# Kernel optimization log

Hardware: AMD Instinct MI355X
Metric: run time of the kernel (lower is better)

## Reference

```python
import jax, jax.numpy as jnp
import numpy as np

N, D, K = 10000, 784, 16          # nodes, input feat dim, num_neighbors
E = N * (K - 1)                   # edges
H = 128                           # hidden width in all MLPs
SIZES = [784, 128, 2]             # node_sizes


def setup_inputs() -> dict:
    key = jax.random.key(0)
    ks = jax.random.split(key, 24)
    w = lambda k, shape: jax.random.normal(k, shape, jnp.float32) * 0.02
    inp = {
        "x": jax.random.normal(ks[0], (N, D), jnp.float32),
        "edge_attr": jax.random.uniform(ks[1], (E, 1), jnp.float32),
        "idxs": jax.random.randint(ks[2], (N, K - 1), 0, N, dtype=jnp.int32),
    }
    # Layer 1: in=784, msg_size=784, out=128
    inp["l1_msg_w1"] = w(ks[3], (D + 1, H));      inp["l1_msg_b1"] = jnp.zeros((H,), jnp.float32)
    inp["l1_msg_w2"] = w(ks[4], (H, D));          inp["l1_msg_b2"] = jnp.zeros((D,), jnp.float32)
    inp["l1_node_w1"] = w(ks[5], (D + D, H));     inp["l1_node_b1"] = jnp.zeros((H,), jnp.float32)
    inp["l1_node_w2"] = w(ks[6], (H, 128));       inp["l1_node_b2"] = jnp.zeros((128,), jnp.float32)
    # Layer 2: in=128, msg_size=128, out=2
    inp["l2_msg_w1"] = w(ks[7], (128 + 1, H));    inp["l2_msg_b1"] = jnp.zeros((H,), jnp.float32)
    inp["l2_msg_w2"] = w(ks[8], (H, 128));        inp["l2_msg_b2"] = jnp.zeros((128,), jnp.float32)
    inp["l2_node_w1"] = w(ks[9], (128 + 128, H)); inp["l2_node_b1"] = jnp.zeros((H,), jnp.float32)
    inp["l2_node_w2"] = w(ks[10], (H, 2));        inp["l2_node_b2"] = jnp.zeros((2,), jnp.float32)
    return inp


def _mlp(x, w1, b1, w2, b2):
    return jax.nn.relu(x @ w1 + b1) @ w2 + b2


def _node_layer(x, src, edge_attr,
                mw1, mb1, mw2, mb2, nw1, nb1, nw2, nb2):
    # message over edges: cat(x[src], edge_attr) -> MLP   [E, msg_size]
    msg = _mlp(jnp.concatenate([x[src], edge_attr], axis=1), mw1, mb1, mw2, mb2)
    # scatter_mean by src index (faithful to the original, which uses index=src)
    sums = jax.ops.segment_sum(msg, src, num_segments=N)
    cnt = jax.ops.segment_sum(jnp.ones((src.shape[0], 1), msg.dtype), src, num_segments=N)
    agg = jnp.where(cnt > 0, sums / jnp.maximum(cnt, 1.0), 0.0)
    # node update: cat(x, agg_msg) -> MLP
    return _mlp(jnp.concatenate([x, agg], axis=1), nw1, nb1, nw2, nb2)


def reference(x, edge_attr, idxs,
              l1_msg_w1, l1_msg_b1, l1_msg_w2, l1_msg_b2,
              l1_node_w1, l1_node_b1, l1_node_w2, l1_node_b2,
              l2_msg_w1, l2_msg_b1, l2_msg_w2, l2_msg_b2,
              l2_node_w1, l2_node_b1, l2_node_w2, l2_node_b2):
    src = idxs.reshape(-1)  # [E]; dst is unused by the original message computation
    h = _node_layer(x, src, edge_attr,
                    l1_msg_w1, l1_msg_b1, l1_msg_w2, l1_msg_b2,
                    l1_node_w1, l1_node_b1, l1_node_w2, l1_node_b2)
    proj = _node_layer(h, src, edge_attr,
                       l2_msg_w1, l2_msg_b1, l2_msg_w2, l2_msg_b2,
                       l2_node_w1, l2_node_b1, l2_node_w2, l2_node_b2)  # [N, 2]
    # vectorized per-neighbor squared distances (replaces the nested python loop)
    neigh = proj[idxs]                                   # [N, K-1, 2]
    d = jnp.sum((proj[:, None, :] - neigh) ** 2, axis=-1)  # [N, K-1]
    return d.reshape(-1, 1)                              # [N*(K-1), 1]
```

## Files before the change

kernel.cpp:

```cpp
#include <hip/hip_runtime.h>

#define N_NODES 10000
#define E_EDGES 150000
#define KNB     15
#define EBLOCKS 587
#define GEMMB   1252
#define KPAD    800
#define PLSTR   204800

typedef unsigned short u16;
typedef __bf16 bf16x8 __attribute__((ext_vector_type(8)));
typedef float  f32x4  __attribute__((ext_vector_type(4)));

__device__ __forceinline__ void split3(float a, u16& h, u16& m, u16& l) {
    unsigned u = __float_as_uint(a);
    unsigned t = u + 0x7FFFu + ((u >> 16) & 1u);
    h = (u16)(t >> 16);
    float r1 = a - __uint_as_float(t & 0xFFFF0000u);
    unsigned u1 = __float_as_uint(r1);
    m = (u16)(u1 >> 16);
    float r2 = r1 - __uint_as_float(u1 & 0xFFFF0000u);
    l = (u16)(__float_as_uint(r2) >> 16);
}

__device__ __forceinline__ void gl_lds16(const u16* g, u16* l) {
    __builtin_amdgcn_global_load_lds(
        (const __attribute__((address_space(1))) unsigned int*)(g),
        (__attribute__((address_space(3))) unsigned int*)(l),
        16, 0, 0);
}

__global__ void count_kernel(const int* __restrict__ idxs, int* __restrict__ cnt, int e) {
    int i = blockIdx.x * blockDim.x + threadIdx.x;
    if (i < e) atomicAdd(&cnt[idxs[i]], 1);
}

__device__ __forceinline__
void gemm_tile2(const float* __restrict__ A, int K,
                const float* __restrict__ Blo, const float* __restrict__ Bhi, int ldB,
                float* __restrict__ C, int ldC, int M,
                int rowBlk, int colBlk) {
    __shared__ float As2[16][34];
    __shared__ float Bs2[16][64];
    int tid = threadIdx.x;
    int tn  = tid & 15, tm = tid >> 4;
    int arow = tid >> 3, acB = (tid & 7) << 1;
    int brow = tid >> 4, bcol = (tid & 15) << 2;
    int rowBase = rowBlk * 32, colBase = colBlk * 64;

    bool half = (Bhi != nullptr) && (colBase >= 128);
    const float* B = half ? Bhi : Blo;
    int bj = colBase - (half ? 128 : 0) + bcol;

    float2 av; float4 bv;
    auto loadA = [&](int k0, float2& dst) {
        int gr = rowBase + arow;
        if (gr < M) dst = *(const float2*)(A + (size_t)gr * K + k0 + acB);
        else { dst.x = dst.y = 0.f; }
    };
    auto loadB = [&](int k0, float4& dst) {
        dst = *(const float4*)(B + (size_t)(k0 + brow) * ldB + bj);
    };
    loadA(0, av); loadB(0, bv);

    float acc[2][4] = {};
    for (int k0 = 0; k0 < K; k0 += 16) {
        __syncthreads();
        As2[acB + 0][arow] = av.x; As2[acB + 1][arow] = av.y;
        *(float4*)&Bs2[brow][bcol] = bv;
        __syncthreads();
        if (k0 + 16 < K) { loadA(k0 + 16, av); loadB(k0 + 16, bv); }
#pragma unroll
        for (int k = 0; k < 16; ++k) {
            float4 b = *(const float4*)&Bs2[k][tn << 2];
            float2 a = *(const float2*)&As2[k][tm << 1];
            acc[0][0] = fmaf(a.x, b.x, acc[0][0]); acc[0][1] = fmaf(a.x, b.y, acc[0][1]);
            acc[0][2] = fmaf(a.x, b.z, acc[0][2]); acc[0][3] = fmaf(a.x, b.w, acc[0][3]);
            acc[1][0] = fmaf(a.y, b.x, acc[1][0]); acc[1][1] = fmaf(a.y, b.y, acc[1][1]);
            acc[1][2] = fmaf(a.y, b.z, acc[1][2]); acc[1][3] = fmaf(a.y, b.w, acc[1][3]);
        }
    }
#pragma unroll
    for (int i = 0; i < 2; ++i) {
        int row = rowBase + tm * 2 + i;
        if (row >= M) continue;
#pragma unroll
        for (int j = 0; j < 4; ++j)
            C[(size_t)row * ldC + colBase + (tn << 2) + j] = acc[i][j];
    }
}

__global__ __launch_bounds__(256)
void scanfold_kernel(const float* __restrict__ mw2, const float* __restrict__ mb2,
                     const float* __restrict__ nw1, const float* __restrict__ nb2,
                     const float* __restrict__ nw2,
                     const float* __restrict__ m2w1, const float* __restrict__ m2b1,
                     const float* __restrict__ m2w2, const float* __restrict__ m2b2,
                     const float* __restrict__ n2w1, const float* __restrict__ n2b1,
                     float* __restrict__ M1, float* __restrict__ M2,
                     float* __restrict__ WH,
                     float* __restrict__ v1, float* __restrict__ v2,
                     float* __restrict__ bu2, float* __restrict__ bx2,
                     const int* __restrict__ cnt, int* __restrict__ eoff,
                     float* __restrict__ maskv, int* __restrict__ fillc,
                     const float* __restrict__ mw1, u16* __restrict__ Bt) {
    int b = blockIdx.x;
    if (b >= 41) {
        __shared__ float Lt[KPAD][17];
        int b2 = b - 41;
        int colBase = b2 * 16;
        const float* S = (colBase < 128) ? mw1 : nw1;
        int sc = colBase & 127;
        int tid = threadIdx.x;
        for (int i = 0; i < 50; ++i) {
            int row = (tid >> 4) + i * 16;
            Lt[row][tid & 15] = (row < 784) ? S[(size_t)row * 128 + sc + (tid & 15)] : 0.f;
        }
        __syncthreads();
        int col = tid >> 4, o = tid & 15;
        size_t dbase = (size_t)(colBase + col) * KPAD;
        for (int o2 = o; o2 < 100; o2 += 16) {
            u16 hs[8], ms[8], ls[8];
#pragma unroll
            for (int e = 0; e < 8; ++e) split3(Lt[o2 * 8 + e][col], hs[e], ms[e], ls[e]);
            auto pk = [](const u16* s) {
                uint4 v;
                v.x = s[0] | ((unsigned)s[1] << 16); v.y = s[2] | ((unsigned)s[3] << 16);
                v.z = s[4] | ((unsigned)s[5] << 16); v.w = s[6] | ((unsigned)s[7] << 16);
                return v;
            };
            *(uint4*)(Bt +           dbase + o2 * 8) = pk(hs);
            *(uint4*)(Bt + PLSTR   + dbase + o2 * 8) = pk(ms);
            *(uint4*)(Bt + 2*PLSTR + dbase + o2 * 8) = pk(ls);
        }
        return;
    }
    if (b == 0) {
        __shared__ int ssum[256];
        int tid = threadIdx.x;
        const int CH = 40;
        int base = tid * CH;
        int v[CH]; int s = 0;
#pragma unroll
        for (int q = 0; q < CH; ++q) {
            int i = base + q;
            v[q] = (i < N_NODES) ? cnt[i] : 0;
            s += v[q];
        }
        ssum[tid] = s;
        __syncthreads();
        for (int off = 1; off < 256; off <<= 1) {
            int t = (tid >= off) ? ssum[tid - off] : 0;
            __syncthreads();
            ssum[tid] += t;
            __syncthreads();
        }
        int ex = ssum[tid] - s;
#pragma unroll
        for (int q = 0; q < CH; ++q) {
            int i = base + q;
            if (i < N_NODES) {
                eoff[i]  = ex;
                maskv[i] = (v[q] > 0) ? 1.f : 0.f;
                fillc[i] = 0;
                ex += v[q];
            }
        }
        return;
    }
    b -= 1;
    if (b < 8) {
        gemm_tile2(mw2, 784, nw1 + 784 * 128, nullptr, 128, M1, 128, 128, b >> 1, b & 1);
    } else if (b < 16) {
        int t = b - 8;
        gemm_tile2(m2w2, 128, n2w1 + 128 * 128, nullptr, 128, M2, 128, 128, t >> 1, t & 1);
    } else if (b < 32) {
        int t = b - 16;
        gemm_tile2(nw2, 128, m2w1, n2w1, 128, WH, 256, 128, t >> 2, t & 3);
    } else {
        __shared__ float red[256];
        int t  = (b - 32) >> 1;
        int j  = ((b - 32) & 1) * 64 + (threadIdx.x & 63);
        int kq = threadIdx.x >> 6;
        const float* bvec; const float* Bv; const float* add; float* out; int Kv;
        if (t == 0)      { bvec = mb2;  Bv = nw1 + 784 * 128;  add = nullptr; out = v1;  Kv = 784; }
        else if (t == 1) { bvec = m2b2; Bv = n2w1 + 128 * 128; add = nullptr; out = v2;  Kv = 128; }
        else if (t == 2) { bvec = nb2;  Bv = m2w1;             add = m2b1;    out = bu2; Kv = 128; }
        else             { bvec = nb2;  Bv = n2w1;             add = n2b1;    out = bx2; Kv = 128; }
        float acc = 0.f;
        for (int k = kq; k < Kv; k += 4) acc = fmaf(bvec[k], Bv[k * 128 + j], acc);
        red[threadIdx.x] = acc;
        __syncthreads();
        if (threadIdx.x < 64) {
            float tot = red[threadIdx.x] + red[threadIdx.x + 64] +
                        red[threadIdx.x + 128] + red[threadIdx.x + 192];
            out[j] = tot + (add ? add[j] : 0.f);
        }
    }
}

#define MF(a, b, c) __builtin_amdgcn_mfma_f32_16x16x32_bf16((a), (b), (c), 0, 0, 0)

__device__ __forceinline__
void gemm_mfma(const float* __restrict__ A, const u16* __restrict__ Bt,
               const float* __restrict__ biasLo, const float* __restrict__ biasHi,
               const float* __restrict__ vhi, const float* __restrict__ rowmask,
               float* __restrict__ C, int gb) {
    __shared__ u16 As[3][2][64][8];
    __shared__ u16 Bs[3][4][64][8];
    const int tid  = threadIdx.x;
    const int lane = tid & 63, w = tid >> 6;
    const int rb = gb >> 2, cbq = gb & 3;
    const int rowBase = rb * 32, colBase = cbq * 64;
    const bool hi = cbq >= 2;
    u16* const AsB = &As[0][0][0][0];
    u16* const BsB = &Bs[0][0][0][0];

    const int srf   = w & 1;
    const int chunk = ((w >> 1) << 2) + (lane >> 4);
    const int aoff  = chunk << 2;
    int arow = rowBase + srf * 16 + (lane & 15);
    if (arow > N_NODES - 1) arow = N_NODES - 1;
    const float* Ap = A + (size_t)arow * 784;
    u16* aDst = AsB + srf * 512 + (((lane & 15) + ((chunk >> 1) << 4)) << 3)
                    + ((chunk & 1) << 2);

#define BSRC(c) ((size_t)((c) >> 2) * PLSTR + \
                 (size_t)(colBase + (((c) & 3) << 4) + (lane & 15)) * KPAD + \
                 ((lane >> 4) << 3))
    const int c0 = w * 3, c1 = w * 3 + 1, c2 = w * 3 + 2;
    const u16* bsrc0 = Bt + BSRC(c0);
    const u16* bsrc1 = Bt + BSRC(c1);
    const u16* bsrc2 = Bt + BSRC(c2);
    u16* bd0 = BsB + c0 * 512;
    u16* bd1 = BsB + c1 * 512;
    u16* bd2 = BsB + c2 * 512;
#undef BSRC

    float4 av;
    ushort4 a3h, a3m, a3l;

#define ALOAD(k0) { int kk = (k0) + aoff; \
    if (kk < 784) av = *(const float4*)(Ap + kk); \
    else { av.x = av.y = av.z = av.w = 0.f; } }
#define ASPLIT() { u16 h, m, l; \
    split3(av.x, h, m, l); a3h.x = h; a3m.x = m; a3l.x = l; \
    split3(av.y, h, m, l); a3h.y = h; a3m.y = m; a3l.y = l; \
    split3(av.z, h, m, l); a3h.z = h; a3m.z = m; a3l.z = l; \
    split3(av.w, h, m, l); a3h.w = h; a3m.w = m; a3l.w = l; }

    f32x4 acc0 = {0.f, 0.f, 0.f, 0.f};
    f32x4 acc1 = acc0;

    const u16* aFr = AsB + (lane << 3);
    const u16* bFr = BsB + (w << 9) + (lane << 3);

    ALOAD(0) ASPLIT()

    for (int t = 0; t < 25; ++t) {
        __syncthreads();
        const int k0 = t << 5;
        gl_lds16(bsrc0 + k0, bd0);
        gl_lds16(bsrc1 + k0, bd1);
        gl_lds16(bsrc2 + k0, bd2);
        *(ushort4*)(aDst)        = a3h;
        *(ushort4*)(aDst + 1024) = a3m;
        *(ushort4*)(aDst + 2048) = a3l;
        __syncthreads();
        if (t < 24) ALOAD((t + 1) << 5)
        {
            bf16x8 a0h = *(const bf16x8*)(aFr);
            bf16x8 a1h = *(const bf16x8*)(aFr + 512);
            bf16x8 a0m = *(const bf16x8*)(aFr + 1024);
            bf16x8 a1m = *(const bf16x8*)(aFr + 1536);
            bf16x8 a0l = *(const bf16x8*)(aFr + 2048);
            bf16x8 a1l = *(const bf16x8*)(aFr + 2560);
            bf16x8 bh  = *(const bf16x8*)(bFr);
            bf16x8 bm  = *(const bf16x8*)(bFr + 2048);
            bf16x8 bl  = *(const bf16x8*)(bFr + 4096);
            acc0 = MF(a0h, bh, acc0); acc1 = MF(a1h, bh, acc1);
            acc0 = MF(a0m, bh, acc0); acc1 = MF(a1m, bh, acc1);
            acc0 = MF(a0l, bh, acc0); acc1 = MF(a1l, bh, acc1);
            acc0 = MF(a0h, bm, acc0); acc1 = MF(a1h, bm, acc1);
            acc0 = MF(a0m, bm, acc0); acc1 = MF(a1m, bm, acc1);
            acc0 = MF(a0h, bl, acc0); acc1 = MF(a1h, bl, acc1);
        }
        if (t < 24) ASPLIT()
    }
#undef ALOAD
#undef ASPLIT

    const float* bias = hi ? biasHi : biasLo;
#define EPI(rf, ACC) { \
        const int col = colBase + w * 16 + (lane & 15); \
        const int cj  = col & 127; \
        const float bb = bias[cj]; \
        const float vh = hi ? vhi[cj] : 0.f; \
        const int rbase = rowBase + (rf) * 16 + ((lane >> 4) << 2); \
        _Pragma("unroll") \
        for (int rr = 0; rr < 4; ++rr) { \
            int row = rbase + rr; \
            if (row < N_NODES) { \
                float v = ACC[rr] + bb; \
                if (hi) v = fmaf(rowmask[row], vh, v); \
                C[(size_t)row * 256 + col] = v; \
            } } }
    EPI(0, acc0) EPI(1, acc1)
#undef EPI
}

__global__ __launch_bounds__(256, 8)
void fillgemm_kernel(const int* __restrict__ idxs, const float* __restrict__ ea,
                     const int* __restrict__ eoff, int* __restrict__ fillc,
                     float* __restrict__ eas,
                     const float* __restrict__ A, const u16* __restrict__ Bt,
                     const float* __restrict__ biasLo, const float* __restrict__ biasHi,
                     const float* __restrict__ vhi, const float* __restrict__ rowmask,
                     float* __restrict__ C) {
    int gb = blockIdx.x;
    if (gb < GEMMB) {
        gemm_mfma(A, Bt, biasLo, biasHi, vhi, rowmask, C, gb);
        return;
    }
    int i = (gb - GEMMB) * 256 + threadIdx.x;
    if (i < E_EDGES) {
        int s = idxs[i];
        int p = atomicAdd(&fillc[s], 1);
        eas[eoff[s] + p] = ea[i];
    }
}

__global__ __launch_bounds__(512, 4)
void tail16_kernel(const float* __restrict__ UX1, const float* __restrict__ w1last,
                   const float* __restrict__ eas, const int* __restrict__ eoff,
                   const int* __restrict__ cnt, const float* __restrict__ maskv,
                   const float* __restrict__ M1, const float* __restrict__ WH,
                   const float* __restrict__ bu2, const float* __restrict__ bx2,
                   const float* __restrict__ v2,
                   const float* __restrict__ w2last, const float* __restrict__ M2,
                   const float* __restrict__ pw, const float* __restrict__ pb,
                   float* __restrict__ UX2, float* __restrict__ proj) {
    __shared__ float Bs[16][264];
    __shared__ float mhT[128][18];
    __shared__ float ts[16][132];
    __shared__ float ebuf[1024];
    int rowBase = blockIdx.x * 16;
    int tid = threadIdx.x;
    int tr  = tid >> 5;
    int tn  = tid & 31;
    int c4  = tn << 2;

    auto msg_phase = [&](const float* __restrict__ U, const float* __restrict__ wl) {
        int d = tid & 127, grp = tid >> 7;
        float w = wl[d];
        float uu[4], sum[4];
        int es[4], ec[4];
#pragma unroll
        for (int it = 0; it < 4; ++it) {
            int n  = rowBase + it * 4 + grp;
            ec[it] = cnt[n];
            es[it] = eoff[n];
            uu[it] = U[(size_t)n * 256 + d];
            sum[it] = 0.f;
        }
        int ebase = eoff[rowBase];
        int eend  = (rowBase + 16 < N_NODES) ? eoff[rowBase + 16] : E_EDGES;
        for (int w0 = ebase; w0 < eend; w0 += 1024) {
            int wlen = min(1024, eend - w0);
            __syncthreads();
            for (int q = tid; q < wlen; q += 512) ebuf[q] = eas[w0 + q];
            __syncthreads();
#pragma unroll
            for (int it = 0; it < 4; ++it) {
                int lo = max(es[it], w0), hiE = min(es[it] + ec[it], w0 + wlen);
                for (int e = lo; e < hiE; ++e)
                    sum[it] += fmaxf(fmaf(ebuf[e - w0], w, uu[it]), 0.f);
            }
        }
#pragma unroll
        for (int it = 0; it < 4; ++it)
            mhT[d][it * 4 + grp] = (ec[it] > 0) ? sum[it] / (float)ec[it] : 0.f;
    };

    msg_phase(UX1, w1last);

    {
        float a0 = 0.f, a1 = 0.f, a2 = 0.f, a3 = 0.f;
        float4 bv = *(const float4*)(M1 + (size_t)tr * 128 + c4);
        for (int k0 = 0; k0 < 128; k0 += 16) {
            __syncthreads();
            *(float4*)&Bs[tr][c4] = bv;
            __syncthreads();
            if (k0 + 16 < 128)
                bv = *(const float4*)(M1 + (size_t)(k0 + 16 + tr) * 128 + c4);
#pragma unroll
            for (int k = 0; k < 16; ++k) {
                float a = mhT[k0 + k][tr];
                float4 b = *(const float4*)&Bs[k][c4];
                a0 = fmaf(a, b.x, a0); a1 = fmaf(a, b.y, a1);
                a2 = fmaf(a, b.z, a2); a3 = fmaf(a, b.w, a3);
            }
        }
        int row = rowBase + tr;
        float4 xn = *(const float4*)(UX1 + (size_t)row * 256 + 128 + c4);
        float4 o;
        o.x = fmaxf(a0 + xn.x, 0.f);
        o.y = fmaxf(a1 + xn.y, 0.f);
        o.z = fmaxf(a2 + xn.z, 0.f);
        o.w = fmaxf(a3 + xn.w, 0.f);
        *(float4*)&ts[tr][c4] = o;
    }

    {
        float u0 = 0.f, u1 = 0.f, u2 = 0.f, u3 = 0.f;
        float x0 = 0.f, x1 = 0.f, x2 = 0.f, x3 = 0.f;
        int c8 = tn << 3;
        float4 bva = *(const float4*)(WH + (size_t)tr * 256 + c8);
        float4 bvb = *(const float4*)(WH + (size_t)tr * 256 + c8 + 4);
        for (int k0 = 0; k0 < 128; k0 += 16) {
            __syncthreads();
            *(float4*)&Bs[tr][c8]     = bva;
            *(float4*)&Bs[tr][c8 + 4] = bvb;
            __syncthreads();
            if (k0 + 16 < 128) {
                bva = *(const float4*)(WH + (size_t)(k0 + 16 + tr) * 256 + c8);
                bvb = *(const float4*)(WH + (size_t)(k0 + 16 + tr) * 256 + c8 + 4);
            }
#pragma unroll
            for (int k = 0; k < 16; ++k) {
                float a = ts[tr][k0 + k];
                float4 b0 = *(const float4*)&Bs[k][c4];
                float4 b1 = *(const float4*)&Bs[k][c4 + 128];
                u0 = fmaf(a, b0.x, u0); u1 = fmaf(a, b0.y, u1);
                u2 = fmaf(a, b0.z, u2); u3 = fmaf(a, b0.w, u3);
                x0 = fmaf(a, b1.x, x0); x1 = fmaf(a, b1.y, x1);
                x2 = fmaf(a, b1.z, x2); x3 = fmaf(a, b1.w, x3);
            }
        }
        int row = rowBase + tr;
        float rm = maskv[row];
        float4 o0, o1;
        o0.x = u0 + bu2[c4 + 0]; o0.y = u1 + bu2[c4 + 1];
        o0.z = u2 + bu2[c4 + 2]; o0.w = u3 + bu2[c4 + 3];
        o1.x = fmaf(rm, v2[c4 + 0], x0 + bx2[c4 + 0]);
        o1.y = fmaf(rm, v2[c4 + 1], x1 + bx2[c4 + 1]);
        o1.z = fmaf(rm, v2[c4 + 2], x2 + bx2[c4 + 2]);
        o1.w = fmaf(rm, v2[c4 + 3], x3 + bx2[c4 + 3]);
        float* orow = UX2 + (size_t)row * 256;
        *(float4*)(orow + c4)       = o0;
        *(float4*)(orow + 128 + c4) = o1;
    }
    __syncthreads();

    msg_phase(UX2, w2last);

    {
        float a0 = 0.f, a1 = 0.f, a2 = 0.f, a3 = 0.f;
        float4 bv = *(const float4*)(M2 + (size_t)tr * 128 + c4);
        for (int k0 = 0; k0 < 128; k0 += 16) {
            __syncthreads();
            *(float4*)&Bs[tr][c4] = bv;
            __syncthreads();
            if (k0 + 16 < 128)
                bv = *(const float4*)(M2 + (size_t)(k0 + 16 + tr) * 128 + c4);
#pragma unroll
            for (int k = 0; k < 16; ++k) {
                float a = mhT[k0 + k][tr];
                float4 b = *(const float4*)&Bs[k][c4];
                a0 = fmaf(a, b.x, a0); a1 = fmaf(a, b.y, a1);
                a2 = fmaf(a, b.z, a2); a3 = fmaf(a, b.w, a3);
            }
        }
        int row = rowBase + tr;
        float4 xn = *(const float4*)(UX2 + (size_t)row * 256 + 128 + c4);
        float t0 = fmaxf(a0 + xn.x, 0.f);
        float t1 = fmaxf(a1 + xn.y, 0.f);
        float t2 = fmaxf(a2 + xn.z, 0.f);
        float t3 = fmaxf(a3 + xn.w, 0.f);
        float pp0 = fmaf(t3, pw[2*(c4+3)],   fmaf(t2, pw[2*(c4+2)],   fmaf(t1, pw[2*(c4+1)],   t0 * pw[2*c4])));
        float pp1 = fmaf(t3, pw[2*(c4+3)+1], fmaf(t2, pw[2*(c4+2)+1], fmaf(t1, pw[2*(c4+1)+1], t0 * pw[2*c4+1])));
        for (int off = 16; off > 0; off >>= 1) {
            pp0 += __shfl_xor(pp0, off, 64);
            pp1 += __shfl_xor(pp1, off, 64);
        }
        if (tn == 0) {
            proj[2 * row]     = pp0 + pb[0];
            proj[2 * row + 1] = pp1 + pb[1];
        }
    }
}

__global__ void dist_kernel(const float* __restrict__ proj, const int* __restrict__ idxs,
                            float* __restrict__ out, int e) {
    int i = blockIdx.x * blockDim.x + threadIdx.x;
    if (i >= e) return;
    int n = i / KNB;
    int m = idxs[i];
    float2 pn = *(const float2*)(proj + 2 * n);
    float2 pm = *(const float2*)(proj + 2 * m);
    float dx = pn.x - pm.x;
    float dy = pn.y - pm.y;
    out[i] = dx * dx + dy * dy;
}

extern "C" void kernel_launch(void* const* d_in, const int* in_sizes, int n_in,
                              void* d_out, int out_size, void* d_ws, size_t ws_size,
                              hipStream_t stream) {
    (void)in_sizes; (void)n_in; (void)out_size; (void)ws_size;
    const float* x    = (const float*)d_in[0];
    const float* eatt = (const float*)d_in[1];
    const int*   idxs = (const int*)d_in[2];
    const float* mw1  = (const float*)d_in[3];
    const float* mb1  = (const float*)d_in[4];
    const float* mw2  = (const float*)d_in[5];
    const float* mb2  = (const float*)d_in[6];
    const float* nw1  = (const float*)d_in[7];
    const float* nb1  = (const float*)d_in[8];
    const float* nw2  = (const float*)d_in[9];
    const float* nb2  = (const float*)d_in[10];
    const float* m2w1 = (const float*)d_in[11];
    const float* m2b1 = (const float*)d_in[12];
    const float* m2w2 = (const float*)d_in[13];
    const float* m2b2 = (const float*)d_in[14];
    const float* n2w1 = (const float*)d_in[15];
    const float* n2b1 = (const float*)d_in[16];
    const float* n2w2 = (const float*)d_in[17];
    const float* n2b2 = (const float*)d_in[18];
    float* out = (float*)d_out;

    float* fws   = (float*)d_ws;
    float* UX1   = fws;
    float* UX2   = fws + 2560000;
    float* proj  = fws + 5120000;
    float* maskv = fws + 5140000;
    float* eas   = fws + 5150016;
    float* M1    = fws + 5300016;
    float* M2    = fws + 5316400;
    float* WH    = fws + 5332784;
    float* v1    = fws + 5365552;
    float* v2    = fws + 5365680;
    float* bu2   = fws + 5365808;
    float* bx2   = fws + 5365936;
    int*   cnt   = (int*)(fws + 5366064);
    int*   fillc = cnt + N_NODES;
    int*   eoff  = fillc + N_NODES;
    u16*   Bt    = (u16*)(fws + 2560000);

    hipMemsetAsync(cnt, 0, N_NODES * sizeof(int), stream);
    count_kernel<<<EBLOCKS, 256, 0, stream>>>(idxs, cnt, E_EDGES);

    scanfold_kernel<<<57, 256, 0, stream>>>(mw2, mb2, nw1, nb2, nw2,
                                            m2w1, m2b1, m2w2, m2b2, n2w1, n2b1,
                                            M1, M2, WH, v1, v2, bu2, bx2,
                                            cnt, eoff, maskv, fillc, mw1, Bt);

    fillgemm_kernel<<<GEMMB + EBLOCKS, 256, 0, stream>>>(
        idxs, eatt, eoff, fillc, eas,
        x, Bt, mb1, nb1, v1, maskv, UX1);

    tail16_kernel<<<625, 512, 0, stream>>>(UX1, mw1 + 784 * 128, eas, eoff, cnt, maskv,
                                           M1, WH, bu2, bx2, v2,
                                           m2w1 + 128 * 128, M2,
                                           n2w2, n2b2,
                                           UX2, proj);

    dist_kernel<<<EBLOCKS, 256, 0, stream>>>(proj, idxs, out, E_EDGES);
}
```

Baseline: 250.8 us.

## Halve GEMM row tile to 16 rows and double GEMM block count

Shrinks the split-bf16 MFMA GEMM tile from 32 to 16 rows per block, doubling the block count to 2500. Each thread now loads and splits two floats per k-step instead of four, and the second accumulator is removed. The aim is more parallelism and less per-block latency, at the cost of reloading B tiles twice as often and doing fewer MFMAs per barrier. Row bounds checks are dropped, which is safe because 10000 is divisible by 16.

```diff
diff --git a/kernel.cpp b/kernel.cpp
--- a/kernel.cpp
+++ b/kernel.cpp
@@ -4,7 +4,7 @@
 #define E_EDGES 150000
 #define KNB     15
 #define EBLOCKS 587
-#define GEMMB   1252
+#define GEMMB   2500
 #define KPAD    800
 #define PLSTR   204800
 
@@ -206,24 +206,20 @@
                const float* __restrict__ biasLo, const float* __restrict__ biasHi,
                const float* __restrict__ vhi, const float* __restrict__ rowmask,
                float* __restrict__ C, int gb) {
-    __shared__ u16 As[3][2][64][8];
+    __shared__ u16 As[3][64][8];
     __shared__ u16 Bs[3][4][64][8];
     const int tid  = threadIdx.x;
     const int lane = tid & 63, w = tid >> 6;
     const int rb = gb >> 2, cbq = gb & 3;
-    const int rowBase = rb * 32, colBase = cbq * 64;
+    const int rowBase = rb * 16, colBase = cbq * 64;
     const bool hi = cbq >= 2;
-    u16* const AsB = &As[0][0][0][0];
+    u16* const AsB = &As[0][0][0];
     u16* const BsB = &Bs[0][0][0][0];
 
-    const int srf   = w & 1;
-    const int chunk = ((w >> 1) << 2) + (lane >> 4);
-    const int aoff  = chunk << 2;
-    int arow = rowBase + srf * 16 + (lane & 15);
-    if (arow > N_NODES - 1) arow = N_NODES - 1;
-    const float* Ap = A + (size_t)arow * 784;
-    u16* aDst = AsB + srf * 512 + (((lane & 15) + ((chunk >> 1) << 4)) << 3)
-                    + ((chunk & 1) << 2);
+    const int srow = tid & 15, kd = tid >> 4;
+    const int aoff = kd << 1;
+    const float* Ap = A + (size_t)(rowBase + srow) * 784;
+    u16* aDst = AsB + ((srow + ((kd >> 2) << 4)) << 3) + ((kd << 1) & 7);
 
 #define BSRC(c) ((size_t)((c) >> 2) * PLSTR + \
                  (size_t)(colBase + (((c) & 3) << 4) + (lane & 15)) * KPAD + \
@@ -237,20 +233,17 @@
     u16* bd2 = BsB + c2 * 512;
 #undef BSRC
 
-    float4 av;
-    ushort4 a3h, a3m, a3l;
+    float2 av;
+    ushort2 a3h, a3m, a3l;
 
 #define ALOAD(k0) { int kk = (k0) + aoff; \
-    if (kk < 784) av = *(const float4*)(Ap + kk); \
-    else { av.x = av.y = av.z = av.w = 0.f; } }
+    if (kk < 784) av = *(const float2*)(Ap + kk); \
+    else { av.x = av.y = 0.f; } }
 #define ASPLIT() { u16 h, m, l; \
     split3(av.x, h, m, l); a3h.x = h; a3m.x = m; a3l.x = l; \
-    split3(av.y, h, m, l); a3h.y = h; a3m.y = m; a3l.y = l; \
-    split3(av.z, h, m, l); a3h.z = h; a3m.z = m; a3l.z = l; \
-    split3(av.w, h, m, l); a3h.w = h; a3m.w = m; a3l.w = l; }
+    split3(av.y, h, m, l); a3h.y = h; a3m.y = m; a3l.y = l; }
 
     f32x4 acc0 = {0.f, 0.f, 0.f, 0.f};
-    f32x4 acc1 = acc0;
 
     const u16* aFr = AsB + (lane << 3);
     const u16* bFr = BsB + (w << 9) + (lane << 3);
@@ -263,27 +256,24 @@
         gl_lds16(bsrc0 + k0, bd0);
         gl_lds16(bsrc1 + k0, bd1);
         gl_lds16(bsrc2 + k0, bd2);
-        *(ushort4*)(aDst)        = a3h;
-        *(ushort4*)(aDst + 1024) = a3m;
-        *(ushort4*)(aDst + 2048) = a3l;
+        *(ushort2*)(aDst)        = a3h;
+        *(ushort2*)(aDst + 512)  = a3m;
+        *(ushort2*)(aDst + 1024) = a3l;
         __syncthreads();
         if (t < 24) ALOAD((t + 1) << 5)
         {
-            bf16x8 a0h = *(const bf16x8*)(aFr);
-            bf16x8 a1h = *(const bf16x8*)(aFr + 512);
-            bf16x8 a0m = *(const bf16x8*)(aFr + 1024);
-            bf16x8 a1m = *(const bf16x8*)(aFr + 1536);
-            bf16x8 a0l = *(const bf16x8*)(aFr + 2048);
-            bf16x8 a1l = *(const bf16x8*)(aFr + 2560);
-            bf16x8 bh  = *(const bf16x8*)(bFr);
-            bf16x8 bm  = *(const bf16x8*)(bFr + 2048);
-            bf16x8 bl  = *(const bf16x8*)(bFr + 4096);
-            acc0 = MF(a0h, bh, acc0); acc1 = MF(a1h, bh, acc1);
-            acc0 = MF(a0m, bh, acc0); acc1 = MF(a1m, bh, acc1);
-            acc0 = MF(a0l, bh, acc0); acc1 = MF(a1l, bh, acc1);
-            acc0 = MF(a0h, bm, acc0); acc1 = MF(a1h, bm, acc1);
-            acc0 = MF(a0m, bm, acc0); acc1 = MF(a1m, bm, acc1);
-            acc0 = MF(a0h, bl, acc0); acc1 = MF(a1h, bl, acc1);
+            bf16x8 ah = *(const bf16x8*)(aFr);
+            bf16x8 am = *(const bf16x8*)(aFr + 512);
+            bf16x8 al = *(const bf16x8*)(aFr + 1024);
+            bf16x8 bh = *(const bf16x8*)(bFr);
+            bf16x8 bm = *(const bf16x8*)(bFr + 2048);
+            bf16x8 bl = *(const bf16x8*)(bFr + 4096);
+            acc0 = MF(ah, bh, acc0);
+            acc0 = MF(am, bh, acc0);
+            acc0 = MF(al, bh, acc0);
+            acc0 = MF(ah, bm, acc0);
+            acc0 = MF(am, bm, acc0);
+            acc0 = MF(ah, bl, acc0);
         }
         if (t < 24) ASPLIT()
     }
@@ -291,22 +281,20 @@
 #undef ASPLIT
 
     const float* bias = hi ? biasHi : biasLo;
-#define EPI(rf, ACC) { \
-        const int col = colBase + w * 16 + (lane & 15); \
-        const int cj  = col & 127; \
-        const float bb = bias[cj]; \
-        const float vh = hi ? vhi[cj] : 0.f; \
-        const int rbase = rowBase + (rf) * 16 + ((lane >> 4) << 2); \
-        _Pragma("unroll") \
-        for (int rr = 0; rr < 4; ++rr) { \
-            int row = rbase + rr; \
-            if (row < N_NODES) { \
-                float v = ACC[rr] + bb; \
-                if (hi) v = fmaf(rowmask[row], vh, v); \
-                C[(size_t)row * 256 + col] = v; \
-            } } }
-    EPI(0, acc0) EPI(1, acc1)
-#undef EPI
+    {
+        const int col = colBase + w * 16 + (lane & 15);
+        const int cj  = col & 127;
+        const float bb = bias[cj];
+        const float vh = hi ? vhi[cj] : 0.f;
+        const int rbase = rowBase + ((lane >> 4) << 2);
+#pragma unroll
+        for (int rr = 0; rr < 4; ++rr) {
+            int row = rbase + rr;
+            float v = acc0[rr] + bb;
+            if (hi) v = fmaf(rowmask[row], vh, v);
+            C[(size_t)row * 256 + col] = v;
+        }
+    }
 }
 
 __global__ __launch_bounds__(256, 8)
```

New measurement: 272.3 us. 1.09x slower.
